# Performance work log

Measured on AMD Instinct MI355X. Metric: run time of the kernel, lower is better.

Reference implementation:

```python
import jax, jax.numpy as jnp
import numpy as np

NUM_HEAD = 16
EMBED_DIM = 1024
HEAD_DIM = EMBED_DIM // NUM_HEAD
QK_DIM = EMBED_DIM  # qk_dim defaults to embed_dim


def setup_inputs() -> dict:
    key = jax.random.key(0)
    k1, k2, k3 = jax.random.split(key, 3)
    x = jax.random.normal(k1, (4, 2048, EMBED_DIM), dtype=jnp.float32)
    # xavier_uniform-like init scale
    lim_qkv = float(np.sqrt(6.0 / (EMBED_DIM + 3 * EMBED_DIM)))
    lim_out = float(np.sqrt(6.0 / (EMBED_DIM + EMBED_DIM)))
    W_QKV = jax.random.uniform(k2, (EMBED_DIM, 3 * EMBED_DIM), jnp.float32, -lim_qkv, lim_qkv)
    W_Out = jax.random.uniform(k3, (EMBED_DIM, EMBED_DIM), jnp.float32, -lim_out, lim_out)
    return {"x": x, "W_QKV": W_QKV, "W_Out": W_Out}


def reference(x, W_QKV, W_Out):
    bsz, slen, _ = x.shape
    # [b,s,3E] -> [b,s,H,hd,3] -> [b,H,s,hd,3]  (interleaved qkv layout, as in torch source)
    qkv = (x @ W_QKV).reshape(bsz, slen, NUM_HEAD, HEAD_DIM, 3).transpose(0, 2, 1, 3, 4)
    q, k, v = qkv[..., 0], qkv[..., 1], qkv[..., 2]
    # NOTE: module scales by sqrt(qk_dim) (full dim), not sqrt(head_dim)
    scores = jnp.einsum("bhqd,bhkd->bhqk", q, k) / np.sqrt(QK_DIM).astype(np.float32)
    attn = jax.nn.softmax(scores, axis=-1)  # dropout p=0.0 -> identity
    out = jnp.einsum("bhqk,bhkd->bhqd", attn, v)  # [b,H,s,hd]
    out = out.transpose(0, 2, 1, 3).reshape(bsz, slen, EMBED_DIM)
    return out @ W_Out
```

## Files before the change

kernel.cpp:

```cpp
#include <hip/hip_runtime.h>
#include <stdint.h>

typedef __bf16 bf16x8 __attribute__((ext_vector_type(8)));
typedef float f32x4 __attribute__((ext_vector_type(4)));
typedef float f32x16 __attribute__((ext_vector_type(16)));
typedef unsigned short u16x8 __attribute__((ext_vector_type(8)));

#if __has_builtin(__builtin_amdgcn_mfma_f32_32x32x16_bf16)
#define MFMA32(a, b, c) __builtin_amdgcn_mfma_f32_32x32x16_bf16((a), (b), (c), 0, 0, 0)
#else
static __device__ __forceinline__ f32x16 MFMA32(bf16x8, bf16x8, f32x16 c) { return c; }
#endif

#if __has_builtin(__builtin_amdgcn_exp2f)
#define EXP2(x) __builtin_amdgcn_exp2f(x)
#else
#define EXP2(x) exp2f(x)
#endif

#if __has_builtin(__builtin_amdgcn_s_setprio)
#define SETPRIO(n) __builtin_amdgcn_s_setprio(n)
#else
#define SETPRIO(n)
#endif

__device__ __forceinline__ unsigned short f2bf(float f) {
    unsigned int u = __float_as_uint(f);
    u += 0x7fffu + ((u >> 16) & 1u);
    return (unsigned short)(u >> 16);
}

__device__ __forceinline__ int swz64(int row, int c) {
    return (c & 7) | ((((c >> 3) ^ row) & 7) << 3);
}

__device__ __forceinline__ int vperm32(int d, int s) {
    int c8 = ((s >> 5) << 2) | (((s >> 4) & 1) << 1) | ((s >> 2) & 1);
    int intra = (s & 3) | (((s >> 3) & 1) << 2);
    return intra + (((c8 ^ d) & 7) << 3);
}

__device__ __forceinline__ void glds16(const unsigned short* g, unsigned short* l) {
    __builtin_amdgcn_global_load_lds((const __attribute__((address_space(1))) void*)g,
                                     (__attribute__((address_space(3))) void*)l, 16, 0, 0);
}

__device__ __forceinline__ void xcd_remap(int nx, int& bx, int& by) {
    int i = blockIdx.y * nx + blockIdx.x;
    int x = i & 7, l = i >> 3;
    bx = l >> 3;
    by = x * 8 + (l & 7);
}

__device__ __forceinline__ void transpose_body(const float* __restrict__ in,
                                               unsigned short* __restrict__ out,
                                               unsigned short (*tile)[33],
                                               int K, int N, int permute, int nb, int kb) {
    int tx = threadIdx.x & 31, ty = threadIdx.x >> 5;
    #pragma unroll
    for (int r = ty; r < 32; r += 8)
        tile[r][tx] = f2bf(in[(size_t)(kb + r) * N + nb + tx]);
    __syncthreads();
    #pragma unroll
    for (int r = ty; r < 32; r += 8) {
        int n_orig = nb + r, col = kb + tx;
        int row;
        if (permute) {
            int h = n_orig / 192, rem = n_orig - h * 192;
            int d = rem / 3, cc = rem - 3 * d;
            row = cc * 1024 + h * 64 + d;
        } else {
            row = n_orig;
        }
        out[(size_t)row * K + (col & ~63) + swz64(row, col & 63)] = tile[tx][r];
    }
}

__global__ __launch_bounds__(256) void preprocess_kernel(const float* __restrict__ x,
                                                         const float* __restrict__ wqkv,
                                                         const float* __restrict__ wout,
                                                         unsigned short* __restrict__ xb,
                                                         unsigned short* __restrict__ wqkvt,
                                                         unsigned short* __restrict__ woutt) {
    __shared__ unsigned short tile[32][33];
    int bid = blockIdx.x;
    if (bid < 4096) {
        size_t id = (size_t)bid * 256 + threadIdx.x;
        int row = (int)(id >> 7);
        int cid = (int)(id & 127);
        const float4* src = (const float4*)(x + id * 8);
        float4 a = src[0], b = src[1];
        u16x8 o;
        o[0] = f2bf(a.x); o[1] = f2bf(a.y); o[2] = f2bf(a.z); o[3] = f2bf(a.w);
        o[4] = f2bf(b.x); o[5] = f2bf(b.y); o[6] = f2bf(b.z); o[7] = f2bf(b.w);
        int group = cid >> 3, ch = cid & 7;
        *(u16x8*)(xb + (size_t)row * 1024 + group * 64 + (((ch ^ row) & 7) << 3)) = o;
    } else if (bid < 7168) {
        int idx = bid - 4096;
        transpose_body(wqkv, wqkvt, tile, 1024, 3072, 1, (idx % 96) * 32, (idx / 96) * 32);
    } else {
        int idx = bid - 7168;
        transpose_body(wout, woutt, tile, 1024, 1024, 0, (idx % 32) * 32, (idx / 32) * 32);
    }
}

__device__ __forceinline__ void gemm128_mainloop(const unsigned short* __restrict__ A,
                                                 const unsigned short* __restrict__ Bt,
                                                 int mbi, int nbi,
                                                 f32x16 acc[2][2]) {
    __shared__ unsigned short smem[4 * 128 * 64];
    const int t = threadIdx.x, lane = t & 63, w = t >> 6;
    const int wm = w & 1, wn = w >> 1;
    const int l31 = lane & 31, h = lane >> 5;
    const size_t mb = (size_t)mbi, nb = (size_t)nbi;

    const f32x16 z16 = {0.f, 0.f, 0.f, 0.f, 0.f, 0.f, 0.f, 0.f,
                        0.f, 0.f, 0.f, 0.f, 0.f, 0.f, 0.f, 0.f};
    #pragma unroll
    for (int mt = 0; mt < 2; mt++)
        #pragma unroll
        for (int nt = 0; nt < 2; nt++) acc[mt][nt] = z16;

    int coff[4];
    #pragma unroll
    for (int ks = 0; ks < 4; ks++)
        coff[ks] = l31 * 64 + ((((2 * ks + h) ^ l31) & 7) << 3);
    const int aw = wm * 4096, bw = wn * 4096;

    const unsigned short* ap = A + (mb + w * 32 + (lane >> 3)) * 1024 + (lane & 7) * 8;
    const unsigned short* bp = Bt + (nb + w * 32 + (lane >> 3)) * 1024 + (lane & 7) * 8;
    unsigned short* al = smem + w * 2048;
    unsigned short* bl = smem + 16384 + w * 2048;
    auto stage = [&](int reg) {
        #pragma unroll
        for (int c = 0; c < 4; c++) {
            glds16(ap + c * 8192, al + reg * 8192 + c * 512);
            glds16(bp + c * 8192, bl + reg * 8192 + c * 512);
        }
        ap += 64;
        bp += 64;
    };

    auto body = [&](const unsigned short* as, const unsigned short* bs) {
        #pragma unroll
        for (int ks = 0; ks < 4; ks++) {
            bf16x8 a0 = *(const bf16x8*)(as + aw + coff[ks]);
            bf16x8 a1 = *(const bf16x8*)(as + aw + 2048 + coff[ks]);
            bf16x8 b0 = *(const bf16x8*)(bs + bw + coff[ks]);
            bf16x8 b1 = *(const bf16x8*)(bs + bw + 2048 + coff[ks]);
            SETPRIO(1);
            acc[0][0] = MFMA32(a0, b0, acc[0][0]);
            acc[0][1] = MFMA32(a0, b1, acc[0][1]);
            acc[1][0] = MFMA32(a1, b0, acc[1][0]);
            acc[1][1] = MFMA32(a1, b1, acc[1][1]);
            SETPRIO(0);
        }
    };

    const unsigned short* A0 = smem;
    const unsigned short* A1 = smem + 8192;
    const unsigned short* B0 = smem + 16384;
    const unsigned short* B1 = smem + 24576;

    stage(0);
    #pragma unroll 1
    for (int j = 0; j < 7; j++) {
        __syncthreads();
        stage(1);
        body(A0, B0);
        __syncthreads();
        stage(0);
        body(A1, B1);
    }
    __syncthreads();
    stage(1);
    body(A0, B0);
    __syncthreads();
    body(A1, B1);
}

__global__ __launch_bounds__(256) void gemm_qkv_kernel(const unsigned short* __restrict__ A,
                                                       const unsigned short* __restrict__ Bt,
                                                       unsigned short* __restrict__ Qo,
                                                       unsigned short* __restrict__ Ko,
                                                       unsigned short* __restrict__ Vo) {
    int bx, by;
    xcd_remap(24, bx, by);
    f32x16 acc[2][2];
    gemm128_mainloop(A, Bt, by * 128, bx * 128, acc);
    const int lane = threadIdx.x & 63, w = threadIdx.x >> 6;
    const int wm = w & 1, wn = w >> 1;
    const int l31 = lane & 31, h = lane >> 5;
    const int mb = by * 128, nb = bx * 128;
    const int cls = nb >> 10;
    const int hh = ((nb & 1023) >> 6) + wn;
    const float SCALE_Q = 1.4426950408889634f / 32.0f;
    #pragma unroll
    for (int mt = 0; mt < 2; mt++) {
        #pragma unroll
        for (int nt = 0; nt < 2; nt++) {
            #pragma unroll
            for (int reg = 0; reg < 16; reg++) {
                int m = mb + wm * 64 + mt * 32 + (reg & 3) + 8 * (reg >> 2) + 4 * h;
                int b = m >> 11, s = m & 2047;
                int bh = b * 16 + hh;
                int d = nt * 32 + l31;
                float v = acc[mt][nt][reg];
                if (cls == 0)
                    Qo[((size_t)bh * 2048 + s) * 64 + swz64(s, d)] = f2bf(v * SCALE_Q);
                else if (cls == 1)
                    Ko[((size_t)bh * 2048 + s) * 64 + swz64(s, d)] = f2bf(v);
                else
                    Vo[((size_t)bh * 64 + d) * 2048 + (s & ~63) + vperm32(d, s & 63)] = f2bf(v);
            }
        }
    }
}

__global__ __launch_bounds__(256) void gemm_out_kernel(const unsigned short* __restrict__ A,
                                                       const unsigned short* __restrict__ Bt,
                                                       float* __restrict__ C) {
    int bx, by;
    xcd_remap(8, bx, by);
    f32x16 acc[2][2];
    gemm128_mainloop(A, Bt, by * 128, bx * 128, acc);
    const int lane = threadIdx.x & 63, w = threadIdx.x >> 6;
    const int wm = w & 1, wn = w >> 1;
    const int l31 = lane & 31, h = lane >> 5;
    const int mb = by * 128, nb = bx * 128;
    #pragma unroll
    for (int mt = 0; mt < 2; mt++)
        #pragma unroll
        for (int nt = 0; nt < 2; nt++)
            #pragma unroll
            for (int reg = 0; reg < 16; reg++) {
                int m = mb + wm * 64 + mt * 32 + (reg & 3) + 8 * (reg >> 2) + 4 * h;
                int n = nb + wn * 64 + nt * 32 + l31;
                C[(size_t)m * 1024 + n] = acc[mt][nt][reg];
            }
}

__global__ __launch_bounds__(256) void attn_kernel(const unsigned short* __restrict__ Qg,
                                                   const unsigned short* __restrict__ Kg,
                                                   const unsigned short* __restrict__ Vt,
                                                   unsigned short* __restrict__ O) {
    __shared__ unsigned short smem[4 * 64 * 64];
    unsigned short* K0 = smem;
    unsigned short* K1 = smem + 4096;
    unsigned short* V0 = smem + 8192;
    unsigned short* V1 = smem + 12288;
    const int t = threadIdx.x, lane = t & 63, w = t >> 6;
    const int l31 = lane & 31, h = lane >> 5;
    const int i_disp = blockIdx.y * 16 + blockIdx.x;
    const int bh = (i_disp & 7) + 8 * (i_disp >> 7);
    const int q0 = ((i_disp >> 3) & 15) * 128;

    int coff[4];
    #pragma unroll
    for (int i = 0; i < 4; i++)
        coff[i] = l31 * 64 + ((((2 * i + h) ^ l31) & 7) << 3);

    bf16x8 qf[4];
    {
        int row = q0 + w * 32 + l31;
        const unsigned short* qbase = Qg + ((size_t)bh * 2048 + row) * 64;
        #pragma unroll
        for (int step = 0; step < 4; step++)
            qf[step] = *(const bf16x8*)(qbase + ((((2 * step + h) ^ row) & 7) << 3));
    }

    const unsigned short* kgp =
        Kg + ((size_t)bh * 2048 + w * 16 + (lane >> 3)) * 64 + (lane & 7) * 8;
    const unsigned short* vgp =
        Vt + ((size_t)bh * 64 + w * 16 + (lane >> 3)) * 2048 + (lane & 7) * 8;
    unsigned short* kl = smem + (w * 16) * 64;
    auto stage = [&](int reg) {
        #pragma unroll
        for (int c = 0; c < 2; c++) {
            glds16(kgp + c * 512, kl + reg * 4096 + c * 512);
            glds16(vgp + c * 16384, kl + 8192 + reg * 4096 + c * 512);
        }
        kgp += 4096;
        vgp += 64;
    };

    const f32x16 z16 = {0.f, 0.f, 0.f, 0.f, 0.f, 0.f, 0.f, 0.f,
                        0.f, 0.f, 0.f, 0.f, 0.f, 0.f, 0.f, 0.f};
    f32x16 acc0 = z16, acc1 = z16;
    float den = 0.f;

    auto pv32 = [&](const f32x16& sg, const unsigned short* vs, int c0) {
        #pragma unroll
        for (int p = 0; p < 2; p++) {
            float e0 = EXP2(sg[8 * p + 0]);
            float e1 = EXP2(sg[8 * p + 1]);
            float e2 = EXP2(sg[8 * p + 2]);
            float e3 = EXP2(sg[8 * p + 3]);
            float e4 = EXP2(sg[8 * p + 4]);
            float e5 = EXP2(sg[8 * p + 5]);
            float e6 = EXP2(sg[8 * p + 6]);
            float e7 = EXP2(sg[8 * p + 7]);
            den += ((e0 + e1) + (e2 + e3)) + ((e4 + e5) + (e6 + e7));
            bf16x8 pb = {(__bf16)e0, (__bf16)e1, (__bf16)e2, (__bf16)e3,
                         (__bf16)e4, (__bf16)e5, (__bf16)e6, (__bf16)e7};
            bf16x8 vf0 = *(const bf16x8*)(vs + coff[c0 + p]);
            bf16x8 vf1 = *(const bf16x8*)(vs + 2048 + coff[c0 + p]);
            SETPRIO(1);
            acc0 = MFMA32(pb, vf0, acc0);
            acc1 = MFMA32(pb, vf1, acc1);
            SETPRIO(0);
        }
    };

    auto body = [&](const unsigned short* ks, const unsigned short* vs) {
        f32x16 s0, s1;
        {
            bf16x8 ka = *(const bf16x8*)(ks + coff[0]);
            bf16x8 kb = *(const bf16x8*)(ks + 2048 + coff[0]);
            SETPRIO(1);
            s0 = MFMA32(ka, qf[0], z16);
            s1 = MFMA32(kb, qf[0], z16);
            SETPRIO(0);
        }
        #pragma unroll
        for (int step = 1; step < 4; step++) {
            bf16x8 ka = *(const bf16x8*)(ks + coff[step]);
            bf16x8 kb = *(const bf16x8*)(ks + 2048 + coff[step]);
            SETPRIO(1);
            s0 = MFMA32(ka, qf[step], s0);
            s1 = MFMA32(kb, qf[step], s1);
            SETPRIO(0);
        }
        pv32(s0, vs, 0);
        pv32(s1, vs, 2);
    };

    stage(0);
    #pragma unroll 1
    for (int it2 = 0; it2 < 15; it2++) {
        __syncthreads();
        stage(1);
        body(K0, V0);
        __syncthreads();
        stage(0);
        body(K1, V1);
    }
    __syncthreads();
    stage(1);
    body(K0, V0);
    __syncthreads();
    body(K1, V1);

    den += __shfl_xor(den, 32);

    const int b = bh >> 4, hd = bh & 15;
    #pragma unroll
    for (int reg = 0; reg < 16; reg++) {
        int qrl = (reg & 3) + 8 * (reg >> 2) + 4 * h;
        float rd = 1.0f / __shfl(den, qrl);
        int srow = q0 + w * 32 + qrl;
        size_t base = ((size_t)b * 2048 + srow) * 1024 + hd * 64;
        O[base + swz64(srow, l31)] = f2bf(acc0[reg] * rd);
        O[base + swz64(srow, 32 + l31)] = f2bf(acc1[reg] * rd);
    }
}

extern "C" void kernel_launch(void* const* d_in, const int* in_sizes, int n_in,
                              void* d_out, int out_size, void* d_ws, size_t ws_size,
                              hipStream_t stream) {
    (void)in_sizes; (void)n_in; (void)out_size; (void)ws_size;
    const float* x = (const float*)d_in[0];
    const float* wqkv = (const float*)d_in[1];
    const float* wout = (const float*)d_in[2];
    float* out = (float*)d_out;

    const size_t SZ_X = 8388608;
    const size_t SZ_WQKV = 3145728;
    const size_t SZ_WOUT = 1048576;

    unsigned short* ws = (unsigned short*)d_ws;
    unsigned short* xb = ws;
    unsigned short* wqkvt = xb + SZ_X;
    unsigned short* woutt = wqkvt + SZ_WQKV;
    unsigned short* Qa = woutt + SZ_WOUT;
    unsigned short* Ka = Qa + SZ_X;
    unsigned short* Va = Ka + SZ_X;
    unsigned short* attn = Va + SZ_X;

    preprocess_kernel<<<8192, 256, 0, stream>>>(x, wqkv, wout, xb, wqkvt, woutt);
    gemm_qkv_kernel<<<dim3(24, 64), 256, 0, stream>>>(xb, wqkvt, Qa, Ka, Va);
    attn_kernel<<<dim3(16, 64), 256, 0, stream>>>(Qa, Ka, Va, attn);
    gemm_out_kernel<<<dim3(8, 64), 256, 0, stream>>>(attn, woutt, out);
}
```

Measured before the change: 272.0 us.

## Load K and V fragments directly from global memory instead of LDS staging

```diff
diff --git a/kernel.cpp b/kernel.cpp
--- a/kernel.cpp
+++ b/kernel.cpp
@@ -244,21 +244,16 @@
                                                    const unsigned short* __restrict__ Kg,
                                                    const unsigned short* __restrict__ Vt,
                                                    unsigned short* __restrict__ O) {
-    __shared__ unsigned short smem[4 * 64 * 64];
-    unsigned short* K0 = smem;
-    unsigned short* K1 = smem + 4096;
-    unsigned short* V0 = smem + 8192;
-    unsigned short* V1 = smem + 12288;
     const int t = threadIdx.x, lane = t & 63, w = t >> 6;
     const int l31 = lane & 31, h = lane >> 5;
     const int i_disp = blockIdx.y * 16 + blockIdx.x;
     const int bh = (i_disp & 7) + 8 * (i_disp >> 7);
     const int q0 = ((i_disp >> 3) & 15) * 128;
 
-    int coff[4];
+    int offs[4];
     #pragma unroll
     for (int i = 0; i < 4; i++)
-        coff[i] = l31 * 64 + ((((2 * i + h) ^ l31) & 7) << 3);
+        offs[i] = (((2 * i + h) ^ l31) & 7) << 3;
 
     bf16x8 qf[4];
     {
@@ -269,27 +264,17 @@
             qf[step] = *(const bf16x8*)(qbase + ((((2 * step + h) ^ row) & 7) << 3));
     }
 
-    const unsigned short* kgp =
-        Kg + ((size_t)bh * 2048 + w * 16 + (lane >> 3)) * 64 + (lane & 7) * 8;
-    const unsigned short* vgp =
-        Vt + ((size_t)bh * 64 + w * 16 + (lane >> 3)) * 2048 + (lane & 7) * 8;
-    unsigned short* kl = smem + (w * 16) * 64;
-    auto stage = [&](int reg) {
-        #pragma unroll
-        for (int c = 0; c < 2; c++) {
-            glds16(kgp + c * 512, kl + reg * 4096 + c * 512);
-            glds16(vgp + c * 16384, kl + 8192 + reg * 4096 + c * 512);
-        }
-        kgp += 4096;
-        vgp += 64;
-    };
+    const unsigned short* kp0 = Kg + ((size_t)bh * 2048 + l31) * 64;
+    const unsigned short* kp1 = kp0 + 32 * 64;
+    const unsigned short* vp0 = Vt + ((size_t)bh * 64 + l31) * 2048;
+    const unsigned short* vp1 = vp0 + (size_t)32 * 2048;
 
     const f32x16 z16 = {0.f, 0.f, 0.f, 0.f, 0.f, 0.f, 0.f, 0.f,
                         0.f, 0.f, 0.f, 0.f, 0.f, 0.f, 0.f, 0.f};
     f32x16 acc0 = z16, acc1 = z16;
     float den = 0.f;
 
-    auto pv32 = [&](const f32x16& sg, const unsigned short* vs, int c0) {
+    auto pv32 = [&](const f32x16& sg, int c0) {
         #pragma unroll
         for (int p = 0; p < 2; p++) {
             float e0 = EXP2(sg[8 * p + 0]);
@@ -303,8 +288,8 @@
             den += ((e0 + e1) + (e2 + e3)) + ((e4 + e5) + (e6 + e7));
             bf16x8 pb = {(__bf16)e0, (__bf16)e1, (__bf16)e2, (__bf16)e3,
                          (__bf16)e4, (__bf16)e5, (__bf16)e6, (__bf16)e7};
-            bf16x8 vf0 = *(const bf16x8*)(vs + coff[c0 + p]);
-            bf16x8 vf1 = *(const bf16x8*)(vs + 2048 + coff[c0 + p]);
+            bf16x8 vf0 = *(const bf16x8*)(vp0 + offs[c0 + p]);
+            bf16x8 vf1 = *(const bf16x8*)(vp1 + offs[c0 + p]);
             SETPRIO(1);
             acc0 = MFMA32(pb, vf0, acc0);
             acc1 = MFMA32(pb, vf1, acc1);
@@ -312,11 +297,12 @@
         }
     };
 
-    auto body = [&](const unsigned short* ks, const unsigned short* vs) {
+    #pragma unroll 1
+    for (int it = 0; it < 32; ++it) {
         f32x16 s0, s1;
         {
-            bf16x8 ka = *(const bf16x8*)(ks + coff[0]);
-            bf16x8 kb = *(const bf16x8*)(ks + 2048 + coff[0]);
+            bf16x8 ka = *(const bf16x8*)(kp0 + offs[0]);
+            bf16x8 kb = *(const bf16x8*)(kp1 + offs[0]);
             SETPRIO(1);
             s0 = MFMA32(ka, qf[0], z16);
             s1 = MFMA32(kb, qf[0], z16);
@@ -324,32 +310,20 @@
         }
         #pragma unroll
         for (int step = 1; step < 4; step++) {
-            bf16x8 ka = *(const bf16x8*)(ks + coff[step]);
-            bf16x8 kb = *(const bf16x8*)(ks + 2048 + coff[step]);
+            bf16x8 ka = *(const bf16x8*)(kp0 + offs[step]);
+            bf16x8 kb = *(const bf16x8*)(kp1 + offs[step]);
             SETPRIO(1);
             s0 = MFMA32(ka, qf[step], s0);
             s1 = MFMA32(kb, qf[step], s1);
             SETPRIO(0);
         }
-        pv32(s0, vs, 0);
-        pv32(s1, vs, 2);
-    };
-
-    stage(0);
-    #pragma unroll 1
-    for (int it2 = 0; it2 < 15; it2++) {
-        __syncthreads();
-        stage(1);
-        body(K0, V0);
-        __syncthreads();
-        stage(0);
-        body(K1, V1);
-    }
-    __syncthreads();
-    stage(1);
-    body(K0, V0);
-    __syncthreads();
-    body(K1, V1);
+        pv32(s0, 0);
+        pv32(s1, 2);
+        kp0 += 4096;
+        kp1 += 4096;
+        vp0 += 64;
+        vp1 += 64;
+    }
 
     den += __shfl_xor(den, 32);
 
```

After: 322.8 us. +18.7%, slower.
